# Kernel optimization log

Hardware: AMD Instinct MI355X
Metric: run time of the kernel (lower is better)

## Reference

```python
import jax, jax.numpy as jnp
import numpy as np

H, DK, DV = 16, 64, 64

def setup_inputs() -> dict:
    key = jax.random.key(0)
    ks = jax.random.split(key, 5)
    S, E = 2048, 1024
    return {
        "x": jax.random.normal(ks[0], (S, E), jnp.float32),
        "Wq": jax.random.normal(ks[1], (H * DK, E), jnp.float32) * 0.02,
        "Wk": jax.random.normal(ks[2], (H * DK, E), jnp.float32) * 0.02,
        "Wv": jax.random.normal(ks[3], (H * DV, E), jnp.float32) * 0.02,
        "Wo": jax.random.normal(ks[4], (H * DV, H * DV), jnp.float32) * 0.02,
    }

def reference(x, Wq, Wk, Wv, Wo):
    S = x.shape[0]
    # Fused QKV projections (equivalent to per-head Linear with concatenated weights)
    Q = (x @ Wq.T).reshape(S, H, DK).transpose(1, 0, 2)  # [H,S,dk]
    K = (x @ Wk.T).reshape(S, H, DK).transpose(1, 0, 2)  # [H,S,dk]
    V = (x @ Wv.T).reshape(S, H, DV).transpose(1, 0, 2)  # [H,S,dv]
    scale = 1.0 / np.sqrt(DK).astype(np.float32)
    scores = jnp.einsum('hsd,htd->hst', Q, K) * scale    # [H,S,S]
    weights = jax.nn.softmax(scores, axis=-1)
    A = jnp.einsum('hst,htv->hsv', weights, V)           # [H,S,dv]
    A1 = A.transpose(1, 0, 2).reshape(S, H * DV)         # concat heads on last dim
    return A1 @ Wo.T
```

## Files before the change

### kernel.cpp

```cpp
#include <hip/hip_runtime.h>
#include <hip/hip_bf16.h>
#include <stdint.h>

typedef uint16_t u16;
typedef uint32_t u32;
typedef float    f32x4  __attribute__((ext_vector_type(4)));
typedef __bf16   bf16x8 __attribute__((ext_vector_type(8)));
typedef uint16_t u16x8  __attribute__((ext_vector_type(8)));
typedef uint16_t u16x4  __attribute__((ext_vector_type(4)));
typedef uint32_t u32x4  __attribute__((ext_vector_type(4)));

#define HH 16
#define SS 2048
#define EE 1024
#define DD 64

__device__ inline u16 f2bf(float f) {
  uint32_t u = __builtin_bit_cast(uint32_t, f);
  u += 0x7fff + ((u >> 16) & 1);
  return (u16)(u >> 16);
}
__device__ inline float bf2f(u16 b) {
  return __builtin_bit_cast(float, (uint32_t)b << 16);
}

__device__ inline u32 cvtpk(float lo, float hi) {
  u32 r;
  asm("v_cvt_pk_bf16_f32 %0, %1, %2" : "=v"(r) : "v"(lo), "v"(hi));
  return r;
}

__device__ inline void gload_lds16(const void* g, void* l) {
  __builtin_amdgcn_global_load_lds(
      (const __attribute__((address_space(1))) uint32_t*)g,
      (__attribute__((address_space(3))) uint32_t*)l, 16, 0, 0);
}

__global__ __launch_bounds__(256) void convert_kernel(
    const float* __restrict__ x,  const float* __restrict__ wq,
    const float* __restrict__ wk, const float* __restrict__ wv,
    const float* __restrict__ wo,
    u16* __restrict__ xb, u16* __restrict__ wqkvb, u16* __restrict__ wob) {
  const int64_t M1 = 1024 * 1024;
  int64_t e = ((int64_t)blockIdx.x * 256 + threadIdx.x) * 4;
  const float* src; u16* dst; int64_t off;
  if (e < 2 * M1)      { src = x;  dst = xb;           off = e; }
  else if (e < 3 * M1) { src = wq; dst = wqkvb;        off = e - 2 * M1; }
  else if (e < 4 * M1) { src = wk; dst = wqkvb + M1;   off = e - 3 * M1; }
  else if (e < 5 * M1) { src = wv; dst = wqkvb + 2*M1; off = e - 4 * M1; }
  else                 { src = wo; dst = wob;          off = e - 5 * M1; }
  float4 v = *(const float4*)(src + off);
  u16x4 o;
  o[0] = f2bf(v.x); o[1] = f2bf(v.y); o[2] = f2bf(v.z); o[3] = f2bf(v.w);
  *(u16x4*)(dst + off) = o;
}

template <int K, int N, int BN>
__global__ __launch_bounds__(256, 4) void gemm_qkv_kernel(
    const u16* __restrict__ A, const u16* __restrict__ B,
    u16* __restrict__ q_ws, u16* __restrict__ k_ws, u16* __restrict__ vt_ws) {
  constexpr int BM = 64, BK = 64;
  constexpr int NFB = BN / 32;
  constexpr float C2 = 0.18033688f;
  __shared__ __align__(16) u16 As[BM * BK];
  __shared__ __align__(16) u16 Bs[BN * BK];
  const int t = threadIdx.x;
  const int lane = t & 63, w = t >> 6;
  const int wr = w >> 1, wc = w & 1;
  const int fr = lane & 15, fg = lane >> 4;

  const int nwg = gridDim.x * gridDim.y;
  const int bid = blockIdx.y * gridDim.x + blockIdx.x;
  const int swz = (bid & 7) * (nwg >> 3) + (bid >> 3);
  const int m0 = (swz / gridDim.x) * BM, n0 = (swz % gridDim.x) * BN;

  f32x4 acc[2][NFB] = {};

  for (int k0 = 0; k0 < K; k0 += BK) {
#pragma unroll
    for (int it = 0; it < 2; ++it) {
      const int c = t + it * 256, row = c >> 3, sch = (c & 7) ^ (row & 7);
      gload_lds16(A + (int64_t)(m0 + row) * K + k0 + sch * 8,
                  As + (c & ~63) * 8);
    }
#pragma unroll
    for (int it = 0; it < BN * 8 / 256; ++it) {
      const int c = t + it * 256, row = c >> 3, sch = (c & 7) ^ (row & 7);
      gload_lds16(B + (int64_t)(n0 + row) * K + k0 + sch * 8,
                  Bs + (c & ~63) * 8);
    }
    __syncthreads();
    bf16x8 af[2][2], bfr[NFB][2];
#pragma unroll
    for (int mi = 0; mi < 2; ++mi)
#pragma unroll
      for (int kc = 0; kc < 2; ++kc) {
        const int row = wr * 32 + mi * 16 + fr;
        const int cc = (kc * 4 + fg) ^ (row & 7);
        af[mi][kc] = __builtin_bit_cast(bf16x8, *(const u16x8*)&As[row * 64 + cc * 8]);
      }
#pragma unroll
    for (int ni = 0; ni < NFB; ++ni)
#pragma unroll
      for (int kc = 0; kc < 2; ++kc) {
        const int row = wc * (BN / 2) + ni * 16 + fr;
        const int cc = (kc * 4 + fg) ^ (row & 7);
        bfr[ni][kc] = __builtin_bit_cast(bf16x8, *(const u16x8*)&Bs[row * 64 + cc * 8]);
      }
#pragma unroll
    for (int kc = 0; kc < 2; ++kc)
#pragma unroll
      for (int mi = 0; mi < 2; ++mi)
#pragma unroll
        for (int ni = 0; ni < NFB; ++ni)
          acc[mi][ni] = __builtin_amdgcn_mfma_f32_16x16x32_bf16(
              af[mi][kc], bfr[ni][kc], acc[mi][ni], 0, 0, 0);
    __syncthreads();
  }

#pragma unroll
  for (int mi = 0; mi < 2; ++mi)
#pragma unroll
    for (int ni = 0; ni < NFB; ++ni)
#pragma unroll
      for (int r = 0; r < 4; ++r) {
        const int m = m0 + wr * 32 + mi * 16 + fg * 4 + r;
        const int n = n0 + wc * (BN / 2) + ni * 16 + fr;
        const float v = acc[mi][ni][r];
        const int which = n >> 10, nn = n & 1023, h = nn >> 6, d = nn & 63;
        if (which == 0)
          q_ws[((int64_t)h * SS + m) * DD + d] = f2bf(v * C2);
        else if (which == 1)
          k_ws[((int64_t)h * SS + m) * DD + d] = f2bf(v);
        else
          vt_ws[((int64_t)h * DD + d) * SS + m] = f2bf(v);
      }
}

__global__ __launch_bounds__(256, 4) void outproj_kernel(
    const u16* __restrict__ opart, const float* __restrict__ lsum,
    const u16* __restrict__ B, float* __restrict__ Cout) {
  constexpr int K = 1024, N = 1024, BM = 64, BN = 64, BK = 64;
  __shared__ __align__(16) u16 As[BM * BK];
  __shared__ __align__(16) u16 Bs[BN * BK];
  const int t = threadIdx.x;
  const int lane = t & 63, w = t >> 6;
  const int wr = w >> 1, wc = w & 1;
  const int fr = lane & 15, fg = lane >> 4;

  const int nwg = gridDim.x * gridDim.y;
  const int bid = blockIdx.y * gridDim.x + blockIdx.x;
  const int swz = (bid & 7) * (nwg >> 3) + (bid >> 3);
  const int m0 = (swz / gridDim.x) * BM, n0 = (swz % gridDim.x) * BN;

  f32x4 acc[2][2] = {};

  for (int k0 = 0; k0 < K; k0 += BK) {
    const int h = k0 >> 6;
#pragma unroll
    for (int it = 0; it < 2; ++it) {
      const int c = t + it * 256, row = c >> 3, sch = (c & 7) ^ (row & 7);
      gload_lds16(B + (int64_t)(n0 + row) * K + k0 + sch * 8,
                  Bs + (c & ~63) * 8);
    }
#pragma unroll
    for (int it = 0; it < 2; ++it) {
      const int c = t + it * 256, row = c >> 3, sch = (c & 7) ^ (row & 7);
      const int q = m0 + row;
      const int64_t off = ((int64_t)h * SS + q) * DD + sch * 8;
      const u16x8 lo = *(const u16x8*)(opart + off);
      const u16x8 hi = *(const u16x8*)(opart + (int64_t)HH * SS * DD + off);
      const float inv =
          1.0f / (lsum[h * SS + q] + lsum[HH * SS + h * SS + q]);
      u32x4 aw;
#pragma unroll
      for (int j = 0; j < 4; ++j) {
        const float a0 = (bf2f(lo[2 * j]) + bf2f(hi[2 * j])) * inv;
        const float a1 = (bf2f(lo[2 * j + 1]) + bf2f(hi[2 * j + 1])) * inv;
        aw[j] = cvtpk(a0, a1);
      }
      *(u32x4*)&As[c * 8] = aw;
    }
    __syncthreads();
    bf16x8 af[2][2], bfr[2][2];
#pragma unroll
    for (int mi = 0; mi < 2; ++mi)
#pragma unroll
      for (int kc = 0; kc < 2; ++kc) {
        const int row = wr * 32 + mi * 16 + fr;
        const int cc = (kc * 4 + fg) ^ (row & 7);
        af[mi][kc] = __builtin_bit_cast(bf16x8, *(const u16x8*)&As[row * 64 + cc * 8]);
      }
#pragma unroll
    for (int ni = 0; ni < 2; ++ni)
#pragma unroll
      for (int kc = 0; kc < 2; ++kc) {
        const int row = wc * 32 + ni * 16 + fr;
        const int cc = (kc * 4 + fg) ^ (row & 7);
        bfr[ni][kc] = __builtin_bit_cast(bf16x8, *(const u16x8*)&Bs[row * 64 + cc * 8]);
      }
#pragma unroll
    for (int kc = 0; kc < 2; ++kc)
#pragma unroll
      for (int mi = 0; mi < 2; ++mi)
#pragma unroll
        for (int ni = 0; ni < 2; ++ni)
          acc[mi][ni] = __builtin_amdgcn_mfma_f32_16x16x32_bf16(
              af[mi][kc], bfr[ni][kc], acc[mi][ni], 0, 0, 0);
    __syncthreads();
  }

#pragma unroll
  for (int mi = 0; mi < 2; ++mi)
#pragma unroll
    for (int ni = 0; ni < 2; ++ni)
#pragma unroll
      for (int r = 0; r < 4; ++r) {
        const int m = m0 + wr * 32 + mi * 16 + fg * 4 + r;
        const int n = n0 + wc * 32 + ni * 16 + fr;
        Cout[(int64_t)m * N + n] = acc[mi][ni][r];
      }
}

__global__ __launch_bounds__(256, 2) void attn_kernel(
    const u16* __restrict__ q_ws, const u16* __restrict__ k_ws,
    const u16* __restrict__ vt_ws, u16* __restrict__ opart,
    float* __restrict__ lsum) {
  constexpr int NTS = SS / 64 / 2;
  __shared__ __align__(16) u16 lds[16384];
  const int t = threadIdx.x;
  const int lane = t & 63, w = t >> 6;
  const int ql = lane & 15, g = lane >> 4;
  const int h = blockIdx.y, qb = blockIdx.x, sp = blockIdx.z;
  const int kt0 = sp * NTS;
  const int qbase = qb * 128 + w * 32;

  const u16* Qh = q_ws + ((int64_t)h * SS + qbase) * DD;
  const u16* Kh = k_ws + ((int64_t)h * SS + kt0 * 64) * DD;
  const u16* Vh = vt_ws + (int64_t)h * DD * SS + kt0 * 64;

  const int r0 = t >> 3, ch = t & 7, r1 = (t + 256) >> 3;
  const int sch0 = ch ^ (r0 & 7), sch1 = ch ^ (r1 & 7);
  const int64_t ko0 = (int64_t)r0 * DD + sch0 * 8;
  const int64_t ko1 = (int64_t)r1 * DD + sch1 * 8;
  const int64_t vo0 = (int64_t)r0 * SS + sch0 * 8;
  const int64_t vo1 = (int64_t)r1 * SS + sch1 * 8;
  const int dst0 = (t & ~63) * 8, dst1 = dst0 + 2048;

  bf16x8 qfl[2], qfh[2];
#pragma unroll
  for (int dd = 0; dd < 2; ++dd) {
    qfl[dd] = __builtin_bit_cast(
        bf16x8, *(const u16x8*)(Qh + ql * DD + dd * 32 + g * 8));
    qfh[dd] = __builtin_bit_cast(
        bf16x8, *(const u16x8*)(Qh + (ql + 16) * DD + dd * 32 + g * 8));
  }

  u16x8 ov;
#pragma unroll
  for (int j = 0; j < 8; ++j) ov[j] = 0x3F80;
  const bf16x8 onesf = __builtin_bit_cast(bf16x8, ov);

  f32x4 ol[4] = {}, oh[4] = {};
  f32x4 o_ll = {}, o_lh = {};

  auto qk = [&](f32x4 (&sl)[4], f32x4 (&sh)[4], const int kb_) {
    __builtin_amdgcn_s_setprio(1);
#pragma unroll
    for (int kb = 0; kb < 4; ++kb) {
      const int key = kb * 16 + ql;
      f32x4 zl = {}, zh = {};
#pragma unroll
      for (int dd = 0; dd < 2; ++dd) {
        bf16x8 kf = __builtin_bit_cast(
            bf16x8,
            *(const u16x8*)&lds[kb_ * 4096 + key * 64 +
                                (((dd * 4 + g) ^ (ql & 7)) * 8)]);
        zl = __builtin_amdgcn_mfma_f32_16x16x32_bf16(kf, qfl[dd], zl, 0, 0, 0);
        zh = __builtin_amdgcn_mfma_f32_16x16x32_bf16(kf, qfh[dd], zh, 0, 0, 0);
      }
      sl[kb] = zl; sh[kb] = zh;
    }
    __builtin_amdgcn_s_setprio(0);
  };

  auto smpv = [&](f32x4 (&sl)[4], f32x4 (&sh)[4], const int vb_) {
#pragma unroll
    for (int kb = 0; kb < 4; ++kb)
#pragma unroll
      for (int r = 0; r < 4; ++r) {
        sl[kb][r] = exp2f(sl[kb][r]);
        sh[kb][r] = exp2f(sh[kb][r]);
      }
#pragma unroll
    for (int ks = 0; ks < 2; ++ks) {
      u32 xl0 = cvtpk(sl[2 * ks][0], sl[2 * ks][1]);
      u32 xl1 = cvtpk(sl[2 * ks][2], sl[2 * ks][3]);
      u32 yl0 = cvtpk(sl[2 * ks + 1][0], sl[2 * ks + 1][1]);
      u32 yl1 = cvtpk(sl[2 * ks + 1][2], sl[2 * ks + 1][3]);
      asm("v_permlane32_swap_b32 %0, %1" : "+v"(xl0), "+v"(yl0));
      asm("v_permlane16_swap_b32 %0, %1" : "+v"(xl0), "+v"(yl0));
      asm("v_permlane32_swap_b32 %0, %1" : "+v"(xl1), "+v"(yl1));
      asm("v_permlane16_swap_b32 %0, %1" : "+v"(xl1), "+v"(yl1));
      u32x4 awl; awl[0] = xl0; awl[1] = xl1; awl[2] = yl0; awl[3] = yl1;
      const bf16x8 pal = __builtin_bit_cast(bf16x8, awl);
      u32 xh0 = cvtpk(sh[2 * ks][0], sh[2 * ks][1]);
      u32 xh1 = cvtpk(sh[2 * ks][2], sh[2 * ks][3]);
      u32 yh0 = cvtpk(sh[2 * ks + 1][0], sh[2 * ks + 1][1]);
      u32 yh1 = cvtpk(sh[2 * ks + 1][2], sh[2 * ks + 1][3]);
      asm("v_permlane32_swap_b32 %0, %1" : "+v"(xh0), "+v"(yh0));
      asm("v_permlane16_swap_b32 %0, %1" : "+v"(xh0), "+v"(yh0));
      asm("v_permlane32_swap_b32 %0, %1" : "+v"(xh1), "+v"(yh1));
      asm("v_permlane16_swap_b32 %0, %1" : "+v"(xh1), "+v"(yh1));
      u32x4 awh; awh[0] = xh0; awh[1] = xh1; awh[2] = yh0; awh[3] = yh1;
      const bf16x8 pah = __builtin_bit_cast(bf16x8, awh);
      __builtin_amdgcn_s_setprio(1);
      o_ll = __builtin_amdgcn_mfma_f32_16x16x32_bf16(pal, onesf, o_ll, 0, 0, 0);
      o_lh = __builtin_amdgcn_mfma_f32_16x16x32_bf16(pah, onesf, o_lh, 0, 0, 0);
#pragma unroll
      for (int nb = 0; nb < 4; ++nb) {
        const int dv = nb * 16 + ql;
        bf16x8 vf = __builtin_bit_cast(
            bf16x8,
            *(const u16x8*)&lds[8192 + vb_ * 4096 + dv * 64 +
                                (((ks * 4 + g) ^ (ql & 7)) * 8)]);
        ol[nb] = __builtin_amdgcn_mfma_f32_16x16x32_bf16(pal, vf, ol[nb], 0, 0, 0);
        oh[nb] = __builtin_amdgcn_mfma_f32_16x16x32_bf16(pah, vf, oh[nb], 0, 0, 0);
      }
      __builtin_amdgcn_s_setprio(0);
    }
  };

  gload_lds16(Kh + ko0, lds + dst0);
  gload_lds16(Kh + ko1, lds + dst1);

  f32x4 sAl[4], sAh[4], sBl[4], sBh[4];
#pragma unroll
  for (int tt = 0; tt < NTS; ++tt) {
    __syncthreads();
    if (tt + 1 < NTS) {
      const u16* Kn = Kh + (int64_t)(tt + 1) * 64 * DD;
      const int kb = ((tt + 1) & 1) * 4096;
      gload_lds16(Kn + ko0, lds + kb + dst0);
      gload_lds16(Kn + ko1, lds + kb + dst1);
    }
    {
      const u16* Vn = Vh + tt * 64;
      const int vb = 8192 + (tt & 1) * 4096;
      gload_lds16(Vn + vo0, lds + vb + dst0);
      gload_lds16(Vn + vo1, lds + vb + dst1);
    }
    if (tt & 1) {
      qk(sBl, sBh, tt & 1);
      smpv(sAl, sAh, (tt - 1) & 1);
    } else {
      qk(sAl, sAh, tt & 1);
      if (tt > 0) smpv(sBl, sBh, (tt - 1) & 1);
    }
  }
  __syncthreads();
  smpv(sBl, sBh, (NTS - 1) & 1);

  const int64_t rowbase = ((int64_t)sp * HH + h) * SS;
#pragma unroll
  for (int r = 0; r < 4; ++r) {
    const int q = qbase + g * 4 + r;
#pragma unroll
    for (int nb = 0; nb < 4; ++nb) {
      opart[(rowbase + q) * DD + nb * 16 + ql] = f2bf(ol[nb][r]);
      opart[(rowbase + q + 16) * DD + nb * 16 + ql] = f2bf(oh[nb][r]);
    }
  }
  if (ql == 0) {
#pragma unroll
    for (int r = 0; r < 4; ++r) {
      lsum[rowbase + qbase + g * 4 + r] = o_ll[r];
      lsum[rowbase + qbase + 16 + g * 4 + r] = o_lh[r];
    }
  }
}

extern "C" void kernel_launch(void* const* d_in, const int* in_sizes, int n_in,
                              void* d_out, int out_size, void* d_ws, size_t ws_size,
                              hipStream_t stream) {
  const float* x  = (const float*)d_in[0];
  const float* wq = (const float*)d_in[1];
  const float* wk = (const float*)d_in[2];
  const float* wv = (const float*)d_in[3];
  const float* wo = (const float*)d_in[4];
  char* ws = (char*)d_ws;
  const int64_t Mi = 1 << 20;
  u16* xb    = (u16*)(ws + 0 * Mi);
  u16* wqkv  = (u16*)(ws + 4 * Mi);
  u16* wob   = (u16*)(ws + 10 * Mi);
  u16* q_ws  = (u16*)(ws + 12 * Mi);
  u16* k_ws  = (u16*)(ws + 16 * Mi);
  u16* vt    = (u16*)(ws + 20 * Mi);
  u16*   opart = (u16*)(ws + 0 * Mi);
  float* lsv   = (float*)(ws + 8 * Mi);
  float* out = (float*)d_out;

  convert_kernel<<<6144, 256, 0, stream>>>(x, wq, wk, wv, wo, xb, wqkv, wob);

  gemm_qkv_kernel<1024, 3072, 128>
      <<<dim3(3072 / 128, 2048 / 64), 256, 0, stream>>>(
      xb, wqkv, q_ws, k_ws, vt);

  attn_kernel<<<dim3(SS / 128, HH, 2), 256, 0, stream>>>(
      q_ws, k_ws, vt, opart, lsv);

  outproj_kernel<<<dim3(1024 / 64, 2048 / 64), 256, 0, stream>>>(
      opart, lsv, wob, out);
}
```

Before: 81.84 us.

## Fuse fp32-to-bf16 conversion into GEMM tile loads, drop convert kernel

New measurement: 89.12 us. +8.9%, slower.

```diff
diff --git a/kernel.cpp b/kernel.cpp
--- a/kernel.cpp
+++ b/kernel.cpp
@@ -7,7 +7,6 @@
 typedef float    f32x4  __attribute__((ext_vector_type(4)));
 typedef __bf16   bf16x8 __attribute__((ext_vector_type(8)));
 typedef uint16_t u16x8  __attribute__((ext_vector_type(8)));
-typedef uint16_t u16x4  __attribute__((ext_vector_type(4)));
 typedef uint32_t u32x4  __attribute__((ext_vector_type(4)));
 
 #define HH 16
@@ -36,31 +35,21 @@
       (__attribute__((address_space(3))) uint32_t*)l, 16, 0, 0);
 }
 
-__global__ __launch_bounds__(256) void convert_kernel(
-    const float* __restrict__ x,  const float* __restrict__ wq,
-    const float* __restrict__ wk, const float* __restrict__ wv,
-    const float* __restrict__ wo,
-    u16* __restrict__ xb, u16* __restrict__ wqkvb, u16* __restrict__ wob) {
-  const int64_t M1 = 1024 * 1024;
-  int64_t e = ((int64_t)blockIdx.x * 256 + threadIdx.x) * 4;
-  const float* src; u16* dst; int64_t off;
-  if (e < 2 * M1)      { src = x;  dst = xb;           off = e; }
-  else if (e < 3 * M1) { src = wq; dst = wqkvb;        off = e - 2 * M1; }
-  else if (e < 4 * M1) { src = wk; dst = wqkvb + M1;   off = e - 3 * M1; }
-  else if (e < 5 * M1) { src = wv; dst = wqkvb + 2*M1; off = e - 4 * M1; }
-  else                 { src = wo; dst = wob;          off = e - 5 * M1; }
-  float4 v = *(const float4*)(src + off);
-  u16x4 o;
-  o[0] = f2bf(v.x); o[1] = f2bf(v.y); o[2] = f2bf(v.z); o[3] = f2bf(v.w);
-  *(u16x4*)(dst + off) = o;
-}
-
-template <int K, int N, int BN>
+__device__ inline u32x4 ld_cvt8(const float* __restrict__ src) {
+  const float4 v0 = *(const float4*)src;
+  const float4 v1 = *(const float4*)(src + 4);
+  u32x4 aw;
+  aw[0] = cvtpk(v0.x, v0.y); aw[1] = cvtpk(v0.z, v0.w);
+  aw[2] = cvtpk(v1.x, v1.y); aw[3] = cvtpk(v1.z, v1.w);
+  return aw;
+}
+
+template <int K>
 __global__ __launch_bounds__(256, 4) void gemm_qkv_kernel(
-    const u16* __restrict__ A, const u16* __restrict__ B,
+    const float* __restrict__ X, const float* __restrict__ Wq,
+    const float* __restrict__ Wk, const float* __restrict__ Wv,
     u16* __restrict__ q_ws, u16* __restrict__ k_ws, u16* __restrict__ vt_ws) {
-  constexpr int BM = 64, BK = 64;
-  constexpr int NFB = BN / 32;
+  constexpr int BM = 64, BN = 128, BK = 64;
   constexpr float C2 = 0.18033688f;
   __shared__ __align__(16) u16 As[BM * BK];
   __shared__ __align__(16) u16 Bs[BN * BK];
@@ -74,23 +63,26 @@
   const int swz = (bid & 7) * (nwg >> 3) + (bid >> 3);
   const int m0 = (swz / gridDim.x) * BM, n0 = (swz % gridDim.x) * BN;
 
-  f32x4 acc[2][NFB] = {};
+  f32x4 acc[2][4] = {};
 
   for (int k0 = 0; k0 < K; k0 += BK) {
 #pragma unroll
     for (int it = 0; it < 2; ++it) {
       const int c = t + it * 256, row = c >> 3, sch = (c & 7) ^ (row & 7);
-      gload_lds16(A + (int64_t)(m0 + row) * K + k0 + sch * 8,
-                  As + (c & ~63) * 8);
-    }
-#pragma unroll
-    for (int it = 0; it < BN * 8 / 256; ++it) {
+      const u32x4 aw = ld_cvt8(X + (int64_t)(m0 + row) * K + k0 + sch * 8);
+      *(u32x4*)&As[c * 8] = aw;
+    }
+#pragma unroll
+    for (int it = 0; it < 4; ++it) {
       const int c = t + it * 256, row = c >> 3, sch = (c & 7) ^ (row & 7);
-      gload_lds16(B + (int64_t)(n0 + row) * K + k0 + sch * 8,
-                  Bs + (c & ~63) * 8);
+      const int n = n0 + row;
+      const float* src = (n < 1024 ? Wq : (n < 2048 ? Wk : Wv));
+      const u32x4 aw =
+          ld_cvt8(src + (int64_t)(n & 1023) * K + k0 + sch * 8);
+      *(u32x4*)&Bs[c * 8] = aw;
     }
     __syncthreads();
-    bf16x8 af[2][2], bfr[NFB][2];
+    bf16x8 af[2][2], bfr[4][2];
 #pragma unroll
     for (int mi = 0; mi < 2; ++mi)
 #pragma unroll
@@ -100,10 +92,10 @@
         af[mi][kc] = __builtin_bit_cast(bf16x8, *(const u16x8*)&As[row * 64 + cc * 8]);
       }
 #pragma unroll
-    for (int ni = 0; ni < NFB; ++ni)
+    for (int ni = 0; ni < 4; ++ni)
 #pragma unroll
       for (int kc = 0; kc < 2; ++kc) {
-        const int row = wc * (BN / 2) + ni * 16 + fr;
+        const int row = wc * 64 + ni * 16 + fr;
         const int cc = (kc * 4 + fg) ^ (row & 7);
         bfr[ni][kc] = __builtin_bit_cast(bf16x8, *(const u16x8*)&Bs[row * 64 + cc * 8]);
       }
@@ -112,7 +104,7 @@
 #pragma unroll
       for (int mi = 0; mi < 2; ++mi)
 #pragma unroll
-        for (int ni = 0; ni < NFB; ++ni)
+        for (int ni = 0; ni < 4; ++ni)
           acc[mi][ni] = __builtin_amdgcn_mfma_f32_16x16x32_bf16(
               af[mi][kc], bfr[ni][kc], acc[mi][ni], 0, 0, 0);
     __syncthreads();
@@ -121,11 +113,11 @@
 #pragma unroll
   for (int mi = 0; mi < 2; ++mi)
 #pragma unroll
-    for (int ni = 0; ni < NFB; ++ni)
+    for (int ni = 0; ni < 4; ++ni)
 #pragma unroll
       for (int r = 0; r < 4; ++r) {
         const int m = m0 + wr * 32 + mi * 16 + fg * 4 + r;
-        const int n = n0 + wc * (BN / 2) + ni * 16 + fr;
+        const int n = n0 + wc * 64 + ni * 16 + fr;
         const float v = acc[mi][ni][r];
         const int which = n >> 10, nn = n & 1023, h = nn >> 6, d = nn & 63;
         if (which == 0)
@@ -139,7 +131,7 @@
 
 __global__ __launch_bounds__(256, 4) void outproj_kernel(
     const u16* __restrict__ opart, const float* __restrict__ lsum,
-    const u16* __restrict__ B, float* __restrict__ Cout) {
+    const float* __restrict__ Wo, float* __restrict__ Cout) {
   constexpr int K = 1024, N = 1024, BM = 64, BN = 64, BK = 64;
   __shared__ __align__(16) u16 As[BM * BK];
   __shared__ __align__(16) u16 Bs[BN * BK];
@@ -160,8 +152,9 @@
 #pragma unroll
     for (int it = 0; it < 2; ++it) {
       const int c = t + it * 256, row = c >> 3, sch = (c & 7) ^ (row & 7);
-      gload_lds16(B + (int64_t)(n0 + row) * K + k0 + sch * 8,
-                  Bs + (c & ~63) * 8);
+      const u32x4 aw =
+          ld_cvt8(Wo + (int64_t)(n0 + row) * K + k0 + sch * 8);
+      *(u32x4*)&Bs[c * 8] = aw;
     }
 #pragma unroll
     for (int it = 0; it < 2; ++it) {
@@ -390,9 +383,6 @@
   const float* wo = (const float*)d_in[4];
   char* ws = (char*)d_ws;
   const int64_t Mi = 1 << 20;
-  u16* xb    = (u16*)(ws + 0 * Mi);
-  u16* wqkv  = (u16*)(ws + 4 * Mi);
-  u16* wob   = (u16*)(ws + 10 * Mi);
   u16* q_ws  = (u16*)(ws + 12 * Mi);
   u16* k_ws  = (u16*)(ws + 16 * Mi);
   u16* vt    = (u16*)(ws + 20 * Mi);
@@ -400,15 +390,13 @@
   float* lsv   = (float*)(ws + 8 * Mi);
   float* out = (float*)d_out;
 
-  convert_kernel<<<6144, 256, 0, stream>>>(x, wq, wk, wv, wo, xb, wqkv, wob);
-
-  gemm_qkv_kernel<1024, 3072, 128>
+  gemm_qkv_kernel<1024>
       <<<dim3(3072 / 128, 2048 / 64), 256, 0, stream>>>(
-      xb, wqkv, q_ws, k_ws, vt);
+      x, wq, wk, wv, q_ws, k_ws, vt);
 
   attn_kernel<<<dim3(SS / 128, HH, 2), 256, 0, stream>>>(
       q_ws, k_ws, vt, opart, lsv);
 
   outproj_kernel<<<dim3(1024 / 64, 2048 / 64), 256, 0, stream>>>(
-      opart, lsv, wob, out);
-}
+      opart, lsv, wo, out);
+}
```
